# Optimization experiments

Hardware: AMD Instinct MI355X
Metric: run time of the kernel (lower is better)

The kernel has to match this reference:

```python
import jax, jax.numpy as jnp
import numpy as np

N = 100000
E = 1600000
F_IN = 128
F_HID = 128


def gcn_conv(x, src, dst, deg_inv_sqrt, W, b, n_nodes):
    # x: [N, Fin] -> [N, Fout]; symmetric-normalized aggregation with self-loops
    h = x @ W  # [N, Fout]
    norm = deg_inv_sqrt[src] * deg_inv_sqrt[dst]  # [E+N] (self-loops appended)
    msgs = h[src] * norm[:, None]  # [E+N, Fout]
    out = jax.ops.segment_sum(msgs, dst, num_segments=n_nodes)
    return out + b


def setup_inputs() -> dict:
    key = jax.random.key(0)
    k = jax.random.split(key, 8)
    x = jax.random.normal(k[0], (N, F_IN), dtype=jnp.float32)
    edge_index = jax.random.randint(k[1], (2, E), 0, N, dtype=jnp.int32)
    s = 1.0 / np.sqrt(F_IN)
    W1 = jax.random.uniform(k[2], (F_IN, F_HID), jnp.float32, -s, s)
    b1 = jnp.zeros((F_HID,), jnp.float32)
    s2 = 1.0 / np.sqrt(F_HID)
    W2 = jax.random.uniform(k[3], (F_HID, F_HID), jnp.float32, -s2, s2)
    b2 = jnp.zeros((F_HID,), jnp.float32)
    W3 = jax.random.uniform(k[4], (F_HID, 1), jnp.float32, -s2, s2)
    b3 = jnp.zeros((1,), jnp.float32)
    return {"x": x, "edge_index": edge_index, "W1": W1, "b1": b1,
            "W2": W2, "b2": b2, "W3": W3, "b3": b3}


def reference(x, edge_index, W1, b1, W2, b2, W3, b3):
    n = x.shape[0]
    loops = jnp.arange(n, dtype=edge_index.dtype)
    src = jnp.concatenate([edge_index[0], loops])  # add self-loops
    dst = jnp.concatenate([edge_index[1], loops])
    deg = jax.ops.segment_sum(jnp.ones_like(dst, dtype=x.dtype), dst, num_segments=n)
    deg_inv_sqrt = jnp.where(deg > 0, jax.lax.rsqrt(deg), 0.0)

    h = gcn_conv(x, src, dst, deg_inv_sqrt, W1, b1, n)
    h = jax.nn.relu(h)  # dropout is identity at inference
    h = gcn_conv(h, src, dst, deg_inv_sqrt, W2, b2, n)
    h = jax.nn.relu(h)
    h = gcn_conv(h, src, dst, deg_inv_sqrt, W3, b3, n)
    return jax.nn.sigmoid(h)  # [N, 1]
```

## Files before the change

kernel.cpp:

```cpp
#include <hip/hip_runtime.h>
#include <cstdint>
#include <cstddef>

#define NN 100000
#define NE 1600000
#define FD 128
#define NXCD 8
#define RNODES ((NN + NXCD - 1) / NXCD)
#define CAP 208192

typedef int vi4 __attribute__((ext_vector_type(4)));

__device__ __forceinline__ float bf_lo(uint32_t u) { return __uint_as_float(u << 16); }
__device__ __forceinline__ float bf_hi(uint32_t u) { return __uint_as_float(u & 0xffff0000u); }
__device__ __forceinline__ uint32_t bf_pack(float a, float b) {
    uint32_t ua = __float_as_uint(a), ub = __float_as_uint(b);
    ua += 0x7fffu + ((ua >> 16) & 1u);
    ub += 0x7fffu + ((ub >> 16) & 1u);
    return (ua >> 16) | (ub & 0xffff0000u);
}

__global__ __launch_bounds__(256) void k_part(const int* __restrict__ src,
                                              const int* __restrict__ dst,
                                              uint32_t* __restrict__ bkt,
                                              int* __restrict__ bcnt, int e) {
    __shared__ int scnt[8];
    __shared__ int sbase[8];
    if (threadIdx.x < 8) scnt[threadIdx.x] = 0;
    __syncthreads();
    const int base = blockIdx.x * 1024 + threadIdx.x * 4;
    const bool valid = base < e;
    int b_[4]; int r_[4]; uint32_t u_[4];
    if (valid) {
        vi4 d4 = __builtin_nontemporal_load((const vi4*)(dst + base));
        vi4 s4 = __builtin_nontemporal_load((const vi4*)(src + base));
        #pragma unroll
        for (int j = 0; j < 4; ++j) {
            int d = d4[j], s = s4[j];
            int b = d / RNODES;
            b_[j] = b;
            u_[j] = ((uint32_t)(d - b * RNODES) << 17) | (uint32_t)s;
            r_[j] = atomicAdd(&scnt[b], 1);
        }
    }
    __syncthreads();
    if (threadIdx.x < 8)
        sbase[threadIdx.x] = atomicAdd(&bcnt[threadIdx.x], scnt[threadIdx.x]);
    __syncthreads();
    if (valid) {
        #pragma unroll
        for (int j = 0; j < 4; ++j) {
            int b = b_[j];
            bkt[(size_t)b * CAP + sbase[b] + r_[j]] = u_[j];
        }
    }
}

__global__ __launch_bounds__(256) void k_hist2(const uint32_t* __restrict__ bkt,
                                               const int* __restrict__ bcnt,
                                               int* __restrict__ cnt) {
    const int xcd  = blockIdx.x & 7;
    const int blk  = blockIdx.x >> 3;
    const int nblk = (int)(gridDim.x >> 3);
    const int m = bcnt[xcd];
    const uint32_t* B = bkt + (size_t)xcd * CAP;
    const int lo = xcd * RNODES;
    for (int i = blk * 256 + threadIdx.x; i < m; i += nblk * 256)
        atomicAdd(&cnt[lo + (int)(B[i] >> 17)], 1);
}

__global__ __launch_bounds__(1024) void k_scan1(const int* __restrict__ cnt,
                                                int* __restrict__ excl,
                                                int* __restrict__ bsum, int n) {
    __shared__ int sh[1024];
    int i = blockIdx.x * 1024 + threadIdx.x;
    int v = (i < n) ? cnt[i] : 0;
    sh[threadIdx.x] = v;
    __syncthreads();
    for (int off = 1; off < 1024; off <<= 1) {
        int t = (threadIdx.x >= off) ? sh[threadIdx.x - off] : 0;
        __syncthreads();
        sh[threadIdx.x] += t;
        __syncthreads();
    }
    if (i < n) excl[i] = sh[threadIdx.x] - v;
    if (threadIdx.x == 1023) bsum[blockIdx.x] = sh[1023];
}

__global__ void k_scan2(int* __restrict__ bsum, int nb) {
    __shared__ int sh[128];
    int t = threadIdx.x;
    int v = (t < nb) ? bsum[t] : 0;
    sh[t] = v;
    __syncthreads();
    for (int off = 1; off < 128; off <<= 1) {
        int u = (t >= off) ? sh[t - off] : 0;
        __syncthreads();
        sh[t] += u;
        __syncthreads();
    }
    if (t < nb) bsum[t] = sh[t] - v;
}

__global__ void k_scan3(int* __restrict__ excl, const int* __restrict__ bsum,
                        int* __restrict__ cursor, const int* __restrict__ cnt,
                        float* __restrict__ dis, int n, int e) {
    int i = blockIdx.x * blockDim.x + threadIdx.x;
    if (i < n) {
        int v = excl[i] + bsum[i >> 10];
        excl[i] = v;
        cursor[i] = v;
        dis[i] = rsqrtf((float)(cnt[i] + 1));
    }
    if (i == 0) excl[n] = e;
}

__global__ __launch_bounds__(256) void k_fill2(const uint32_t* __restrict__ bkt,
                                               const int* __restrict__ bcnt,
                                               int* __restrict__ cursor,
                                               uint2* __restrict__ colw,
                                               const float* __restrict__ dis) {
    const int xcd  = blockIdx.x & 7;
    const int blk  = blockIdx.x >> 3;
    const int nblk = (int)(gridDim.x >> 3);
    const int m = bcnt[xcd];
    const uint32_t* B = bkt + (size_t)xcd * CAP;
    const int lo = xcd * RNODES;
    for (int i = blk * 256 + threadIdx.x; i < m; i += nblk * 256) {
        uint32_t u = B[i];
        int s = (int)(u & 0x1FFFFu);
        int d = lo + (int)(u >> 17);
        int pos = atomicAdd(&cursor[d], 1);
        uint2 cw;
        cw.x = (uint32_t)s;
        cw.y = __float_as_uint(dis[s] * dis[d]);
        colw[pos] = cw;
    }
}

template <typename TIN>
__global__ __launch_bounds__(256) void k_gemm(const TIN* __restrict__ X,
                                              const float* __restrict__ W,
                                              unsigned short* __restrict__ H, int n) {
    __shared__ float At[64][68];
    __shared__ float Ws[64][64];
    const int t  = threadIdx.x;
    const int tx = t & 15;
    const int ty = t >> 4;
    const int rb = blockIdx.x * 64;
    const int cb = blockIdx.y * 64;

    float acc[4][4] = {};

    for (int c = 0; c < 2; ++c) {
        #pragma unroll
        for (int r = 0; r < 4; ++r) {
            int f   = t + 256 * r;
            int row = f >> 4;
            int kc  = (f & 15) << 2;
            int grow = rb + row;
            float4 v = make_float4(0.f, 0.f, 0.f, 0.f);
            if (grow < n) {
                if constexpr (sizeof(TIN) == 4) {
                    v = *(const float4*)((const float*)X + (size_t)grow * FD + c * 64 + kc);
                } else {
                    uint2 p = *(const uint2*)((const unsigned short*)X + (size_t)grow * FD + c * 64 + kc);
                    v.x = bf_lo(p.x); v.y = bf_hi(p.x);
                    v.z = bf_lo(p.y); v.w = bf_hi(p.y);
                }
            }
            At[kc + 0][row] = v.x;
            At[kc + 1][row] = v.y;
            At[kc + 2][row] = v.z;
            At[kc + 3][row] = v.w;
            *(float4*)&Ws[row][kc] =
                *(const float4*)(W + (size_t)(c * 64 + row) * FD + cb + kc);
        }
        __syncthreads();
        #pragma unroll 8
        for (int k = 0; k < 64; ++k) {
            float4 a = *(const float4*)&At[k][ty * 4];
            float4 b = *(const float4*)&Ws[k][tx * 4];
            acc[0][0] = fmaf(a.x, b.x, acc[0][0]);
            acc[0][1] = fmaf(a.x, b.y, acc[0][1]);
            acc[0][2] = fmaf(a.x, b.z, acc[0][2]);
            acc[0][3] = fmaf(a.x, b.w, acc[0][3]);
            acc[1][0] = fmaf(a.y, b.x, acc[1][0]);
            acc[1][1] = fmaf(a.y, b.y, acc[1][1]);
            acc[1][2] = fmaf(a.y, b.z, acc[1][2]);
            acc[1][3] = fmaf(a.y, b.w, acc[1][3]);
            acc[2][0] = fmaf(a.z, b.x, acc[2][0]);
            acc[2][1] = fmaf(a.z, b.y, acc[2][1]);
            acc[2][2] = fmaf(a.z, b.z, acc[2][2]);
            acc[2][3] = fmaf(a.z, b.w, acc[2][3]);
            acc[3][0] = fmaf(a.w, b.x, acc[3][0]);
            acc[3][1] = fmaf(a.w, b.y, acc[3][1]);
            acc[3][2] = fmaf(a.w, b.z, acc[3][2]);
            acc[3][3] = fmaf(a.w, b.w, acc[3][3]);
        }
        __syncthreads();
    }

    #pragma unroll
    for (int i = 0; i < 4; ++i) {
        int grow = rb + ty * 4 + i;
        if (grow < n) {
            uint2 p;
            p.x = bf_pack(acc[i][0], acc[i][1]);
            p.y = bf_pack(acc[i][2], acc[i][3]);
            *(uint2*)(H + (size_t)grow * FD + cb + tx * 4) = p;
        }
    }
}

template <int MODE>
__global__ __launch_bounds__(256) void k_agg(const unsigned short* __restrict__ h,
                                             const float* __restrict__ dis,
                                             const int* __restrict__ rp,
                                             const uint2* __restrict__ colw,
                                             const float* __restrict__ bias,
                                             const float* __restrict__ W3,
                                             unsigned short* __restrict__ out,
                                             float* __restrict__ outf, int n) {
    const uint32_t* h32 = (const uint32_t*)h;
    int wid  = (int)((blockIdx.x * (size_t)blockDim.x + threadIdx.x) >> 6);
    int lane = threadIdx.x & 63;
    int w2 = __builtin_amdgcn_readfirstlane(wid);
    int i0 = 2 * w2;
    if (i0 >= n) return;
    int i1 = i0 + 1;
    const bool has1 = (i1 < n);

    const int e00 = rp[i0];
    const int e01 = rp[i0 + 1];
    const int e11 = has1 ? rp[i0 + 2] : e01;

    float di0 = dis[i0];
    float di1 = has1 ? dis[i1] : 0.f;
    float2 acc0, acc1;
    {
        uint32_t su0 = h32[(size_t)i0 * 64 + lane];
        float q0 = di0 * di0;
        acc0.x = bf_lo(su0) * q0; acc0.y = bf_hi(su0) * q0;
        if (has1) {
            uint32_t su1 = h32[(size_t)i1 * 64 + lane];
            float q1 = di1 * di1;
            acc1.x = bf_lo(su1) * q1; acc1.y = bf_hi(su1) * q1;
        } else { acc1.x = acc1.y = 0.f; }
    }

    const int ng0 = (e01 - e00 + 15) >> 4;
    const int ng1 = (e11 - e01 + 15) >> 4;
    const int ng  = ng0 > ng1 ? ng0 : ng1;

    for (int g = 0; g < ng; ++g) {
        const bool do0 = (g < ng0), do1 = (g < ng1);
        int s0[16], s1[16];
        float w0_[16], w1_[16];
        uint32_t v0[16], v1[16];
        if (do0) {
            const int jb = e00 + g * 16;
            if (jb + 16 <= e01) {
                #pragma unroll
                for (int q = 0; q < 16; ++q) {
                    uint2 cw = colw[jb + q];
                    s0[q] = (int)cw.x; w0_[q] = __uint_as_float(cw.y);
                }
            } else {
                #pragma unroll
                for (int q = 0; q < 16; ++q) {
                    int idx = jb + q;
                    int c   = idx < e01 ? idx : e01 - 1;
                    uint2 cw = colw[c];
                    s0[q]  = (int)cw.x;
                    w0_[q] = idx < e01 ? __uint_as_float(cw.y) : 0.f;
                }
            }
        }
        if (do1) {
            const int jb = e01 + g * 16;
            if (jb + 16 <= e11) {
                #pragma unroll
                for (int q = 0; q < 16; ++q) {
                    uint2 cw = colw[jb + q];
                    s1[q] = (int)cw.x; w1_[q] = __uint_as_float(cw.y);
                }
            } else {
                #pragma unroll
                for (int q = 0; q < 16; ++q) {
                    int idx = jb + q;
                    int c   = idx < e11 ? idx : e11 - 1;
                    uint2 cw = colw[c];
                    s1[q]  = (int)cw.x;
                    w1_[q] = idx < e11 ? __uint_as_float(cw.y) : 0.f;
                }
            }
        }
        if (do0) {
            #pragma unroll
            for (int q = 0; q < 16; ++q)
                v0[q] = h32[(size_t)s0[q] * 64 + lane];
        }
        if (do1) {
            #pragma unroll
            for (int q = 0; q < 16; ++q)
                v1[q] = h32[(size_t)s1[q] * 64 + lane];
        }
        if (do0) {
            #pragma unroll
            for (int q = 0; q < 16; ++q) {
                acc0.x = fmaf(w0_[q], bf_lo(v0[q]), acc0.x);
                acc0.y = fmaf(w0_[q], bf_hi(v0[q]), acc0.y);
            }
        }
        if (do1) {
            #pragma unroll
            for (int q = 0; q < 16; ++q) {
                acc1.x = fmaf(w1_[q], bf_lo(v1[q]), acc1.x);
                acc1.y = fmaf(w1_[q], bf_hi(v1[q]), acc1.y);
            }
        }
    }

    float2 b = ((const float2*)bias)[lane];
    acc0.x = fmaxf(acc0.x + b.x, 0.f);
    acc0.y = fmaxf(acc0.y + b.y, 0.f);
    acc1.x = fmaxf(acc1.x + b.x, 0.f);
    acc1.y = fmaxf(acc1.y + b.y, 0.f);

    if (MODE == 0) {
        ((uint32_t*)out)[(size_t)i0 * 64 + lane] = bf_pack(acc0.x, acc0.y);
        if (has1)
            ((uint32_t*)out)[(size_t)i1 * 64 + lane] = bf_pack(acc1.x, acc1.y);
    } else {
        float2 w3 = ((const float2*)W3)[lane];
        float d0 = acc0.x * w3.x + acc0.y * w3.y;
        float d1 = acc1.x * w3.x + acc1.y * w3.y;
        #pragma unroll
        for (int off = 32; off; off >>= 1) {
            d0 += __shfl_xor(d0, off);
            d1 += __shfl_xor(d1, off);
        }
        if (lane == 0) {
            outf[i0] = d0;
            if (has1) outf[i1] = d1;
        }
    }
}

__global__ __launch_bounds__(256) void k_agg1(const float* __restrict__ h3,
                                              const float* __restrict__ dis,
                                              const int* __restrict__ rp,
                                              const uint2* __restrict__ colw,
                                              const float* __restrict__ b3,
                                              float* __restrict__ out, int n) {
    int i    = (int)((blockIdx.x * (size_t)blockDim.x + threadIdx.x) >> 6);
    int lane = threadIdx.x & 63;
    if (i >= n) return;
    float di  = dis[i];
    float acc = (lane == 0) ? di * di * h3[i] : 0.f;
    const int e0 = rp[i], e1 = rp[i + 1];
    for (int base = e0 + lane; base < e1; base += 64) {
        uint2 cw = colw[base];
        acc = fmaf(__uint_as_float(cw.y), h3[(int)cw.x], acc);
    }
    #pragma unroll
    for (int off = 32; off; off >>= 1) acc += __shfl_xor(acc, off);
    if (lane == 0) {
        float v = acc + b3[0];
        out[i] = 1.f / (1.f + expf(-v));
    }
}

static inline size_t alg(size_t x) { return (x + 255) & ~(size_t)255; }

extern "C" void kernel_launch(void* const* d_in, const int* in_sizes, int n_in,
                              void* d_out, int out_size, void* d_ws, size_t ws_size,
                              hipStream_t stream) {
    const float* x   = (const float*)d_in[0];
    const int*   ei  = (const int*)d_in[1];
    const float* W1  = (const float*)d_in[2];
    const float* b1  = (const float*)d_in[3];
    const float* W2  = (const float*)d_in[4];
    const float* b2  = (const float*)d_in[5];
    const float* W3  = (const float*)d_in[6];
    const float* b3  = (const float*)d_in[7];
    float*       out = (float*)d_out;

    const int n = NN, e = NE;
    const int* src = ei;
    const int* dst = ei + e;

    char* w = (char*)d_ws;
    float* dis    = (float*)w;  w += alg((size_t)n * 4);
    int*   cnt    = (int*)w;    w += alg((size_t)n * 4);
    int*   bcnt   = (int*)w;    w += alg((size_t)8 * 4);
    int*   rp     = (int*)w;    w += alg((size_t)(n + 1) * 4);
    int*   cursor = (int*)w;    w += alg((size_t)n * 4);
    int*   bsum   = (int*)w;    w += alg((size_t)128 * 4);
    uint32_t* bkt = (uint32_t*)w; w += alg((size_t)NXCD * CAP * 4);
    uint2* colw   = (uint2*)w;  w += alg((size_t)e * 8);
    unsigned short* bufA = (unsigned short*)w; w += alg((size_t)n * FD * 2);
    unsigned short* bufB = (unsigned short*)w; w += alg((size_t)n * FD * 2);
    float* h3     = (float*)w;  w += alg((size_t)n * 4);

    hipMemsetAsync(cnt, 0, (size_t)n * 4, stream);
    hipMemsetAsync(bcnt, 0, 8 * 4, stream);

    const int B = 256;
    const int gN = (n + B - 1) / B;
    const int nScan = (n + 1023) / 1024;
    const int nChunk = (e + 1023) / 1024;

    k_part<<<nChunk, B, 0, stream>>>(src, dst, bkt, bcnt, e);
    k_hist2<<<2048, B, 0, stream>>>(bkt, bcnt, cnt);
    k_scan1<<<nScan, 1024, 0, stream>>>(cnt, rp, bsum, n);
    k_scan2<<<1, 128, 0, stream>>>(bsum, nScan);
    k_scan3<<<gN, B, 0, stream>>>(rp, bsum, cursor, cnt, dis, n, e);
    k_fill2<<<2048, B, 0, stream>>>(bkt, bcnt, cursor, colw, dis);

    dim3 gGemm((n + 63) / 64, 2);
    const int nWave2  = (n + 1) / 2;
    const int gWave2  = (nWave2 * 64 + B - 1) / B;
    const int gWave   = (n * 64 + B - 1) / B;

    k_gemm<float><<<gGemm, B, 0, stream>>>(x, W1, bufA, n);
    k_agg<0><<<gWave2, B, 0, stream>>>(bufA, dis, rp, colw, b1, W3, bufB, h3, n);
    k_gemm<unsigned short><<<gGemm, B, 0, stream>>>(bufB, W2, bufA, n);
    k_agg<1><<<gWave2, B, 0, stream>>>(bufA, dis, rp, colw, b2, W3, bufB, h3, n);
    k_agg1<<<gWave, B, 0, stream>>>(h3, dis, rp, colw, b3, out, n);
}
```

Before: 525.1 us.

## Replace scalar FMA GEMM with bf16 MFMA 16x16x32 matrix-core kernel

Rewrites the dense feature transform to use bf16 MFMA instructions. Each block stages the full 128x128 weight matrix in LDS as transposed bf16, and each wave computes a 16x128 output tile. This removes the scalar FMA inner loop and the two-column grid split, so the A rows are read only once. In exchange, the weights and the fp32 input are rounded to bf16 before the multiply, and the output is written as scattered 2-byte stores.

```diff
diff --git a/kernel.cpp b/kernel.cpp
--- a/kernel.cpp
+++ b/kernel.cpp
@@ -10,6 +10,8 @@
 #define CAP 208192
 
 typedef int vi4 __attribute__((ext_vector_type(4)));
+typedef __attribute__((ext_vector_type(8))) short bf16x8;
+typedef __attribute__((ext_vector_type(4))) float f32x4;
 
 __device__ __forceinline__ float bf_lo(uint32_t u) { return __uint_as_float(u << 16); }
 __device__ __forceinline__ float bf_hi(uint32_t u) { return __uint_as_float(u & 0xffff0000u); }
@@ -18,6 +20,11 @@
     ua += 0x7fffu + ((ua >> 16) & 1u);
     ub += 0x7fffu + ((ub >> 16) & 1u);
     return (ua >> 16) | (ub & 0xffff0000u);
+}
+__device__ __forceinline__ unsigned short bf1(float a) {
+    uint32_t u = __float_as_uint(a);
+    u += 0x7fffu + ((u >> 16) & 1u);
+    return (unsigned short)(u >> 16);
 }
 
 __global__ __launch_bounds__(256) void k_part(const int* __restrict__ src,
@@ -142,74 +149,63 @@
 __global__ __launch_bounds__(256) void k_gemm(const TIN* __restrict__ X,
                                               const float* __restrict__ W,
                                               unsigned short* __restrict__ H, int n) {
-    __shared__ float At[64][68];
-    __shared__ float Ws[64][64];
-    const int t  = threadIdx.x;
-    const int tx = t & 15;
-    const int ty = t >> 4;
-    const int rb = blockIdx.x * 64;
-    const int cb = blockIdx.y * 64;
-
-    float acc[4][4] = {};
-
-    for (int c = 0; c < 2; ++c) {
-        #pragma unroll
-        for (int r = 0; r < 4; ++r) {
-            int f   = t + 256 * r;
-            int row = f >> 4;
-            int kc  = (f & 15) << 2;
-            int grow = rb + row;
-            float4 v = make_float4(0.f, 0.f, 0.f, 0.f);
-            if (grow < n) {
-                if constexpr (sizeof(TIN) == 4) {
-                    v = *(const float4*)((const float*)X + (size_t)grow * FD + c * 64 + kc);
-                } else {
-                    uint2 p = *(const uint2*)((const unsigned short*)X + (size_t)grow * FD + c * 64 + kc);
-                    v.x = bf_lo(p.x); v.y = bf_hi(p.x);
-                    v.z = bf_lo(p.y); v.w = bf_hi(p.y);
-                }
-            }
-            At[kc + 0][row] = v.x;
-            At[kc + 1][row] = v.y;
-            At[kc + 2][row] = v.z;
-            At[kc + 3][row] = v.w;
-            *(float4*)&Ws[row][kc] =
-                *(const float4*)(W + (size_t)(c * 64 + row) * FD + cb + kc);
-        }
-        __syncthreads();
-        #pragma unroll 8
-        for (int k = 0; k < 64; ++k) {
-            float4 a = *(const float4*)&At[k][ty * 4];
-            float4 b = *(const float4*)&Ws[k][tx * 4];
-            acc[0][0] = fmaf(a.x, b.x, acc[0][0]);
-            acc[0][1] = fmaf(a.x, b.y, acc[0][1]);
-            acc[0][2] = fmaf(a.x, b.z, acc[0][2]);
-            acc[0][3] = fmaf(a.x, b.w, acc[0][3]);
-            acc[1][0] = fmaf(a.y, b.x, acc[1][0]);
-            acc[1][1] = fmaf(a.y, b.y, acc[1][1]);
-            acc[1][2] = fmaf(a.y, b.z, acc[1][2]);
-            acc[1][3] = fmaf(a.y, b.w, acc[1][3]);
-            acc[2][0] = fmaf(a.z, b.x, acc[2][0]);
-            acc[2][1] = fmaf(a.z, b.y, acc[2][1]);
-            acc[2][2] = fmaf(a.z, b.z, acc[2][2]);
-            acc[2][3] = fmaf(a.z, b.w, acc[2][3]);
-            acc[3][0] = fmaf(a.w, b.x, acc[3][0]);
-            acc[3][1] = fmaf(a.w, b.y, acc[3][1]);
-            acc[3][2] = fmaf(a.w, b.z, acc[3][2]);
-            acc[3][3] = fmaf(a.w, b.w, acc[3][3]);
-        }
-        __syncthreads();
-    }
-
+    __shared__ unsigned short Wl[128][136];
+    const int t = threadIdx.x;
     #pragma unroll
-    for (int i = 0; i < 4; ++i) {
-        int grow = rb + ty * 4 + i;
-        if (grow < n) {
-            uint2 p;
-            p.x = bf_pack(acc[i][0], acc[i][1]);
-            p.y = bf_pack(acc[i][2], acc[i][3]);
-            *(uint2*)(H + (size_t)grow * FD + cb + tx * 4) = p;
-        }
+    for (int c = 0; c < 16; ++c) {
+        int idx4 = (c * 256 + t) * 4;
+        int k  = idx4 >> 7;
+        int nn = idx4 & 127;
+        float4 v = *(const float4*)(W + idx4);
+        Wl[nn + 0][k] = bf1(v.x);
+        Wl[nn + 1][k] = bf1(v.y);
+        Wl[nn + 2][k] = bf1(v.z);
+        Wl[nn + 3][k] = bf1(v.w);
+    }
+    __syncthreads();
+
+    const int wave = t >> 6, lane = t & 63;
+    const int row0 = blockIdx.x * 64 + wave * 16;
+    if (row0 >= n) return;
+    const int arow = row0 + (lane & 15);
+    const int kb8  = (lane >> 4) * 8;
+
+    bf16x8 a[4];
+    if constexpr (sizeof(TIN) == 4) {
+        const float* Xf = (const float*)X;
+        #pragma unroll
+        for (int kt = 0; kt < 4; ++kt) {
+            const float* p = Xf + (size_t)arow * FD + kt * 32 + kb8;
+            float4 u0 = *(const float4*)p;
+            float4 u1 = *(const float4*)(p + 4);
+            bf16x8 f;
+            f[0] = (short)bf1(u0.x); f[1] = (short)bf1(u0.y);
+            f[2] = (short)bf1(u0.z); f[3] = (short)bf1(u0.w);
+            f[4] = (short)bf1(u1.x); f[5] = (short)bf1(u1.y);
+            f[6] = (short)bf1(u1.z); f[7] = (short)bf1(u1.w);
+            a[kt] = f;
+        }
+    } else {
+        const unsigned short* Xb = (const unsigned short*)X;
+        #pragma unroll
+        for (int kt = 0; kt < 4; ++kt)
+            a[kt] = *(const bf16x8*)(Xb + (size_t)arow * FD + kt * 32 + kb8);
+    }
+
+    const int ccol  = lane & 15;
+    const int crow0 = row0 + (lane >> 4) * 4;
+    #pragma unroll
+    for (int nt = 0; nt < 8; ++nt) {
+        f32x4 acc = {0.f, 0.f, 0.f, 0.f};
+        const int bcol = nt * 16 + (lane & 15);
+        #pragma unroll
+        for (int kt = 0; kt < 4; ++kt) {
+            bf16x8 b = *(const bf16x8*)&Wl[bcol][kt * 32 + kb8];
+            acc = __builtin_amdgcn_mfma_f32_16x16x32_bf16(a[kt], b, acc, 0, 0, 0);
+        }
+        #pragma unroll
+        for (int j = 0; j < 4; ++j)
+            H[(size_t)(crow0 + j) * FD + nt * 16 + ccol] = bf1(acc[j]);
     }
 }
 
@@ -419,7 +415,7 @@
     k_scan3<<<gN, B, 0, stream>>>(rp, bsum, cursor, cnt, dis, n, e);
     k_fill2<<<2048, B, 0, stream>>>(bkt, bcnt, cursor, colw, dis);
 
-    dim3 gGemm((n + 63) / 64, 2);
+    const int gGemm = (n + 63) / 64;
     const int nWave2  = (n + 1) / 2;
     const int gWave2  = (nWave2 * 64 + B - 1) / B;
     const int gWave   = (n * 64 + B - 1) / B;
```

Result: faster. 486.4 us (-7.4%).
